# Kernel optimization log

Hardware: AMD Instinct MI355X
Metric: run time of the kernel (lower is better)

## Reference

```python
import jax, jax.numpy as jnp
import numpy as np

INPUT_SIZE = 512
HIDDEN_SIZE = 1024
OUTPUT_SIZE = 512
BATCH = 64
SEQ = 512


def _xavier(key, shape):
    fan_in, fan_out = shape
    bound = np.sqrt(6.0 / (fan_in + fan_out)).astype(np.float32)
    return jax.random.uniform(key, shape, jnp.float32, -bound, bound)


def setup_inputs() -> dict:
    key = jax.random.key(0)
    ks = jax.random.split(key, 7)
    comb = INPUT_SIZE + HIDDEN_SIZE
    return {
        "x": jax.random.normal(ks[0], (BATCH, SEQ, INPUT_SIZE), jnp.float32),
        "W_i": _xavier(ks[1], (comb, HIDDEN_SIZE)),
        "W_f": _xavier(ks[2], (comb, HIDDEN_SIZE)),
        "W_c": _xavier(ks[3], (comb, HIDDEN_SIZE)),
        "W_o": _xavier(ks[4], (comb, HIDDEN_SIZE)),
        "b_i": jnp.zeros((HIDDEN_SIZE,), jnp.float32),
        "b_f": jnp.zeros((HIDDEN_SIZE,), jnp.float32),
        "b_c": jnp.zeros((HIDDEN_SIZE,), jnp.float32),
        "b_o": jnp.zeros((HIDDEN_SIZE,), jnp.float32),
        "fc_w": _xavier(ks[5], (OUTPUT_SIZE, HIDDEN_SIZE)),  # torch Linear weight [out, in]
        "fc_b": jnp.zeros((OUTPUT_SIZE,), jnp.float32),
    }


def reference(x, W_i, W_f, W_c, W_o, b_i, b_f, b_c, b_o, fc_w, fc_b):
    batch = x.shape[0]
    hidden = W_i.shape[1]
    # Fuse the 4 gate weights into one [in+h, 4h] matrix: single GEMM per step.
    W = jnp.concatenate([W_i, W_f, W_c, W_o], axis=1)  # [in+h, 4h]
    b = jnp.concatenate([b_i, b_f, b_c, b_o], axis=0)  # [4h]

    def step(carry, x_t):
        h, c = carry
        combined = jnp.concatenate([x_t, h], axis=1)        # [B, in+h]
        gates = combined @ W + b                            # [B, 4h]
        i_t, f_t, g_t, o_t = jnp.split(gates, 4, axis=1)
        i_t = jax.nn.sigmoid(i_t)
        f_t = jax.nn.sigmoid(f_t)
        g_t = jnp.tanh(g_t)
        o_t = jax.nn.sigmoid(o_t)
        c = f_t * c + i_t * g_t
        h = o_t * jnp.tanh(c)
        return (h, c), None

    h0 = jnp.zeros((batch, hidden), x.dtype)
    c0 = jnp.zeros((batch, hidden), x.dtype)
    (h_T, _), _ = jax.lax.scan(step, (h0, c0), jnp.swapaxes(x, 0, 1))
    return h_T @ fc_w.T + fc_b  # [B, output_size]
```

## Files before the change

kernel.cpp:

```cpp
#include <hip/hip_runtime.h>

typedef unsigned char u8;
typedef unsigned short u16;
typedef unsigned int u32;
typedef unsigned long long u64;
typedef __attribute__((ext_vector_type(4))) int i32x4;
typedef __attribute__((ext_vector_type(4))) float f32x4;

#define SEQ 512

#define OFF_XBQ  0ull
#define OFF_WXQ  33554432ull
#define OFF_WHQ  35651584ull
#define OFF_SCL  39845888ull
#define OFF_SXG  39878656ull
#define OFF_HIMG 40009728ull
#define OFF_TAG  40271872ull
#define OFF_CTL  40305152ull

__device__ inline u16 f2bf(float f) {
  u32 u = __float_as_uint(f);
  return (u16)((u + 0x7fffu + ((u >> 16) & 1u)) >> 16);
}
__device__ inline float bf2f(u16 u) { return __uint_as_float(((u32)u) << 16); }
__device__ inline float sigm(float x) { return 1.f / (1.f + __expf(-x)); }
__device__ inline float tanh_(float x) { return 1.f - 2.f / (1.f + __expf(2.f * x)); }

#define MFMA_I8(a, b, c_) __builtin_amdgcn_mfma_i32_16x16x64_i8(a, b, c_, 0, 0, 0)

__device__ inline u32 ald32(const u32* p) {
  return __hip_atomic_load(p, __ATOMIC_RELAXED, __HIP_MEMORY_SCOPE_AGENT);
}
__device__ inline void st32_plain(u32* p, u32 v) {
  asm volatile("global_store_dword %0, %1, off" :: "v"(p), "v"(v) : "memory");
}
#define VMWAIT0() asm volatile("s_waitcnt vmcnt(0)" ::: "memory")
#define L1INV()   asm volatile("buffer_inv" ::: "memory")
#define CBAR()    asm volatile("" ::: "memory")

__global__ void pack_xq(const float* __restrict__ x, u8* __restrict__ xbq,
                        float* __restrict__ sxg) {
  __shared__ u8 st[1024];
  const int bid = blockIdx.x;
  const int brow = bid >> 9, tau = bid & 511;
  const int lane = threadIdx.x;
  const float* src = x + ((size_t)bid << 9) + lane * 8;
  float4 a = *(const float4*)src;
  float4 b = *(const float4*)(src + 4);
  float v[8] = {a.x, a.y, a.z, a.w, b.x, b.y, b.z, b.w};
  float m = 0.f;
#pragma unroll
  for (int j = 0; j < 8; ++j) m = fmaxf(m, fabsf(v[j]));
#pragma unroll
  for (int i = 1; i < 64; i <<= 1) m = fmaxf(m, __shfl_xor(m, i));
  m = fmaxf(m, 1e-20f);
  const float s = m * (1.f / 127.f), inv = 127.f / m;
#pragma unroll
  for (int j = 0; j < 8; ++j) {
    float t = v[j] * inv;
    float hi = rintf(t);
    float lo = rintf((t - hi) * 254.f);
    st[lane * 8 + j] = (u8)(signed char)(int)hi;
    st[512 + lane * 8 + j] = (u8)(signed char)(int)lo;
  }
  __syncthreads();
  const int hl = lane >> 5, ks = (lane >> 2) & 7, kg = lane & 3;
  uint4 u = *(const uint4*)&st[hl * 512 + ks * 64 + kg * 16];
  const int c = tau >> 2, tc = tau & 3, g = brow >> 3, rb = brow & 7;
  const int mrow = tc * 8 + rb, mt = mrow >> 4, m15 = mrow & 15;
  *(uint4*)(xbq + (size_t)(((((c * 8 + g) * 2 + hl) * 2 + mt) * 8 + ks) * 64 +
                           kg * 16 + m15) * 16) = u;
  if (lane == 0) sxg[tau * 64 + brow] = s;
}

__global__ void calc_scales(const float* __restrict__ W0, const float* __restrict__ W1,
                            const float* __restrict__ W2, const float* __restrict__ W3,
                            float* __restrict__ scl) {
  const int id = blockIdx.x * 256 + threadIdx.x;
  const int part = id >> 12, q = (id >> 10) & 3, cc = id & 1023;
  const float* Wg = q == 0 ? W0 : q == 1 ? W1 : q == 2 ? W2 : W3;
  const int r0 = part ? 512 : 0, n = part ? 1024 : 512;
  float mx = 1e-8f;
  for (int k = 0; k < n; ++k) mx = fmaxf(mx, fabsf(Wg[(size_t)(r0 + k) * 1024 + cc]));
  scl[id] = mx * (1.f / 127.f);
}

__global__ void pack_whq(const float* __restrict__ W0, const float* __restrict__ W1,
                         const float* __restrict__ W2, const float* __restrict__ W3,
                         const float* __restrict__ scl, u8* __restrict__ whq) {
  const int id = blockIdx.x * 256 + threadIdx.x;
  const int lane = id & 63, ks = (id >> 6) & 15, q = (id >> 10) & 3;
  const int w = (id >> 12) & 1, slot = id >> 13;
  const int hcol = slot * 32 + w * 16 + (lane & 15);
  const float* Wg = q == 0 ? W0 : q == 1 ? W1 : q == 2 ? W2 : W3;
  const int k0 = ks * 64 + (lane >> 4) * 16;
  const float inv_s = 1.f / scl[4096 + q * 1024 + hcol];
  u8 tmp[16];
#pragma unroll
  for (int j = 0; j < 16; ++j) {
    float v = Wg[(size_t)(512 + k0 + j) * 1024 + hcol] * inv_s;
    tmp[j] = (u8)(signed char)(int)rintf(fminf(fmaxf(v, -127.f), 127.f));
  }
  *(uint4*)(whq + (size_t)id * 16) = *(uint4*)tmp;
}

__global__ void pack_wxq(const float* __restrict__ W0, const float* __restrict__ W1,
                         const float* __restrict__ W2, const float* __restrict__ W3,
                         const float* __restrict__ scl, u8* __restrict__ wxq) {
  const int id = blockIdx.x * 256 + threadIdx.x;
  const int lane = id & 63, ks = (id >> 6) & 7, q = (id >> 9) & 3;
  const int w = (id >> 11) & 1, slot = id >> 12;
  const int hcol = slot * 32 + w * 16 + (lane & 15);
  const float* Wg = q == 0 ? W0 : q == 1 ? W1 : q == 2 ? W2 : W3;
  const int k0 = ks * 64 + (lane >> 4) * 16;
  const float inv_s = 1.f / scl[q * 1024 + hcol];
  u8 tmp[16];
#pragma unroll
  for (int j = 0; j < 16; ++j) {
    float v = Wg[(size_t)(k0 + j) * 1024 + hcol] * inv_s;
    tmp[j] = (u8)(signed char)(int)rintf(fminf(fmaxf(v, -127.f), 127.f));
  }
  *(uint4*)(wxq + (size_t)id * 16) = *(uint4*)tmp;
}

__global__ void __launch_bounds__(192, 1) lstm_main(
    char* __restrict__ ws,
    const float* __restrict__ b_i, const float* __restrict__ b_f,
    const float* __restrict__ b_c, const float* __restrict__ b_o,
    const float* __restrict__ fcw, const float* __restrict__ fcb,
    float* __restrict__ out) {
  __shared__ __align__(16) u8 wh[131072];
  __shared__ __align__(16) u16 ring_[8192];
  __shared__ __align__(16) u8 pub_[512];
  __shared__ u32 flg[16];

  const int tid = threadIdx.x;
  const int wid = tid >> 6;
  const int lane = tid & 63;
  const int kgrp = lane >> 4;
  const int l15 = lane & 15;

  u32 xcd;
  asm volatile("s_getreg_b32 %0, hwreg(HW_REG_XCC_ID, 0, 8)" : "=s"(xcd));
  const int g = (int)(xcd & 7);

  if (tid == 0) {
    u32 s = __hip_atomic_fetch_add((u32*)(ws + OFF_CTL) + g * 16, 1u,
                                   __ATOMIC_RELAXED, __HIP_MEMORY_SCOPE_SYSTEM);
    flg[0] = s; flg[1] = 0; flg[2] = 0; flg[3] = 0;
  }
  __syncthreads();
  const int slot = (int)flg[0];
  if (slot >= 32) return;

  u8* himg = (u8*)(ws + OFF_HIMG) + (size_t)g * 32768;
  u32* tags = (u32*)(ws + OFF_TAG) + g * 1024;
  const float* scl = (const float*)(ws + OFF_SCL);

  {
    const u8* src = (const u8*)(ws + OFF_WHQ) + (size_t)slot * 131072;
    for (int i = 0; i < 43; ++i) {
      int u = i * 192 + tid;
      if (u < 8192) *(uint4*)&wh[u * 16] = *(const uint4*)(src + u * 16);
    }
  }
  __syncthreads();

  if (wid == 2) {
    const u8* xq = (const u8*)(ws + OFF_XBQ);
    const u8* wxs = (const u8*)(ws + OFF_WXQ) + (size_t)slot * 65536;
    const float* sxg = (const float*)(ws + OFF_SXG);
    float swx[2][4], bs[2][4];
#pragma unroll
    for (int w2 = 0; w2 < 2; ++w2) {
      const int cwq = slot * 32 + w2 * 16 + l15;
#pragma unroll
      for (int q = 0; q < 4; ++q) swx[w2][q] = scl[q * 1024 + cwq];
      bs[w2][0] = b_i[cwq]; bs[w2][1] = b_f[cwq];
      bs[w2][2] = b_c[cwq]; bs[w2][3] = b_o[cwq];
    }
    for (int c = 0; c < 128; ++c) {
      if (c >= 2) {
        const u32 need = (u32)(4 * c - 4);
        while (((volatile u32*)flg)[2] < need || ((volatile u32*)flg)[3] < need) {}
        CBAR();
      }
      float sxv[2][4];
#pragma unroll
      for (int mt = 0; mt < 2; ++mt)
#pragma unroll
        for (int r = 0; r < 4; ++r)
          sxv[mt][r] = sxg[(c * 4 + mt * 2 + (kgrp >> 1)) * 64 + g * 8 + (kgrp & 1) * 4 + r];
      i32x4 accH[2][2][4], accL[2][2][4];
#pragma unroll
      for (int mt = 0; mt < 2; ++mt)
#pragma unroll
        for (int w2 = 0; w2 < 2; ++w2)
#pragma unroll
          for (int q = 0; q < 4; ++q) {
            accH[mt][w2][q] = (i32x4){0, 0, 0, 0};
            accL[mt][w2][q] = (i32x4){0, 0, 0, 0};
          }
      const u8* xc = xq + (size_t)(c * 8 + g) * 32768;
#pragma unroll 2
      for (int ks = 0; ks < 8; ++ks) {
        i32x4 aH0 = *(const i32x4*)(xc + (size_t)((0 * 2 + 0) * 8 + ks) * 1024 + lane * 16);
        i32x4 aH1 = *(const i32x4*)(xc + (size_t)((0 * 2 + 1) * 8 + ks) * 1024 + lane * 16);
        i32x4 aL0 = *(const i32x4*)(xc + (size_t)((1 * 2 + 0) * 8 + ks) * 1024 + lane * 16);
        i32x4 aL1 = *(const i32x4*)(xc + (size_t)((1 * 2 + 1) * 8 + ks) * 1024 + lane * 16);
#pragma unroll
        for (int w2 = 0; w2 < 2; ++w2)
#pragma unroll
          for (int q = 0; q < 4; ++q) {
            i32x4 b = *(const i32x4*)(wxs + (size_t)(((w2 * 4 + q) * 8 + ks) * 64 + lane) * 16);
            accH[0][w2][q] = MFMA_I8(aH0, b, accH[0][w2][q]);
            accH[1][w2][q] = MFMA_I8(aH1, b, accH[1][w2][q]);
            accL[0][w2][q] = MFMA_I8(aL0, b, accL[0][w2][q]);
            accL[1][w2][q] = MFMA_I8(aL1, b, accL[1][w2][q]);
          }
      }
#pragma unroll
      for (int mt = 0; mt < 2; ++mt)
#pragma unroll
        for (int w2 = 0; w2 < 2; ++w2)
#pragma unroll
          for (int q = 0; q < 4; ++q) {
            u64 pk = 0;
#pragma unroll
            for (int r = 0; r < 4; ++r) {
              float val = sxv[mt][r] * swx[w2][q] *
                          ((float)accH[mt][w2][q][r] + (float)accL[mt][w2][q][r] * (1.f / 254.f)) +
                          bs[w2][q];
              pk |= (u64)f2bf(val) << (16 * r);
            }
            const int tc = mt * 2 + (kgrp >> 1);
            const int cc2 = (w2 * 4 + q) * 16 + l15;
            const int rb0 = (kgrp & 1) * 4;
            *(u64*)&ring_[(((c & 1) * 4 + tc) * 128 + cc2) * 8 + rb0] = pk;
          }
      asm volatile("s_waitcnt lgkmcnt(0)" ::: "memory");
      ((volatile u32*)flg)[1] = (u32)(c + 1);
    }
    return;
  }

  const int w = wid;
  const int col = slot * 32 + w * 16 + l15;
  const int idx = slot * 2 + w;
  float sA[4];
#pragma unroll
  for (int q = 0; q < 4; ++q) sA[q] = scl[4096 + q * 1024 + col] * (1.f / 127.f);

  float cs[4] = {0.f, 0.f, 0.f, 0.f};
  u32* mytag = tags + idx * 16;
  const volatile u32* mypoll = (const volatile u32*)(tags + lane * 16);
  const int rbb = (kgrp & 1) * 4;

  for (int t = 1; t <= SEQ; ++t) {
    const int tau = t - 1, ch = tau >> 2, tc = tau & 3, par = tau & 1;
    while (((volatile u32*)flg)[1] <= (u32)ch) {}
    CBAR();
    f32x4 gx[4];
#pragma unroll
    for (int q = 0; q < 4; ++q) {
      u64 pk = *(const u64*)&ring_[(((ch & 1) * 4 + tc) * 128 + (w * 4 + q) * 16 + l15) * 8 + rbb];
      gx[q][0] = bf2f((u16)pk);         gx[q][1] = bf2f((u16)(pk >> 16));
      gx[q][2] = bf2f((u16)(pk >> 32)); gx[q][3] = bf2f((u16)(pk >> 48));
    }
    const u8* ab = himg + par * 16384 + lane * 16;
    u32 spins = 0;
    u64 rb = __ballot(*mypoll >= (u32)tau);
    i32x4 A[16];
    i32x4 acc[4];
#pragma unroll
    for (int q = 0; q < 4; ++q) acc[q] = (i32x4){0, 0, 0, 0};
#pragma unroll
    for (int q4 = 0; q4 < 4; ++q4) {
      const u64 need = 0xFFFFull << (q4 * 16);
      while ((rb & need) != need) {
        u32 v = (++spins > (1u << 20)) ? ald32((const u32*)mypoll) : *mypoll;
        rb = __ballot(v >= (u32)tau);
      }
      CBAR();
      L1INV();
#pragma unroll
      for (int k4 = 0; k4 < 4; ++k4)
        A[q4 * 4 + k4] = *(const i32x4*)(ab + (size_t)(q4 * 4 + k4) * 1024);
      if (q4 > 0) {
#pragma unroll
        for (int k4 = 0; k4 < 4; ++k4) {
          const int ks = (q4 - 1) * 4 + k4;
#pragma unroll
          for (int q = 0; q < 4; ++q) {
            i32x4 b = *(const i32x4*)&wh[(size_t)(((w * 4 + q) * 16 + ks) * 64 + lane) * 16];
            acc[q] = MFMA_I8(A[ks], b, acc[q]);
          }
        }
      }
    }
#pragma unroll
    for (int k4 = 0; k4 < 4; ++k4) {
      const int ks = 12 + k4;
#pragma unroll
      for (int q = 0; q < 4; ++q) {
        i32x4 b = *(const i32x4*)&wh[(size_t)(((w * 4 + q) * 16 + ks) * 64 + lane) * 16];
        acc[q] = MFMA_I8(A[ks], b, acc[q]);
      }
    }
#pragma unroll
    for (int r = 0; r < 4; ++r) {
      float p[4];
#pragma unroll
      for (int q = 0; q < 4; ++q) {
        float hiF = (float)acc[q][r];
        float loF = (float)__shfl_xor(acc[q][r], 32);
        p[q] = fmaf(sA[q], fmaf(loF, 1.f / 254.f, hiF), gx[q][r]);
      }
      float iv = sigm(p[0]), fv = sigm(p[1]), gv = tanh_(p[2]), ov = sigm(p[3]);
      float cn = fv * cs[r] + iv * gv;
      cs[r] = cn;
      float h = ov * tanh_(cn);
      float hq = h * 127.f;
      float hi = rintf(hq);
      float lo = rintf((hq - hi) * 254.f);
      if (kgrp < 2) {
        const int rr = kgrp * 4 + r;
        pub_[w * 256 + rr * 16 + l15] = (u8)(signed char)(int)hi;
        pub_[w * 256 + (8 + rr) * 16 + l15] = (u8)(signed char)(int)lo;
      }
    }
    asm volatile("s_waitcnt lgkmcnt(0)" ::: "memory");
    if (lane < 16) {
      uint4 v = *(const uint4*)&pub_[w * 256 + lane * 16];
      u8* dst = himg + (size_t)((t & 1) * 16384) +
                (size_t)(((idx >> 2) * 64 + (idx & 3) * 16 + lane) * 16);
      *(uint4*)dst = v;
    }
    VMWAIT0();
    if (lane == 0) st32_plain(mytag, (u32)t);
    ((volatile u32*)flg)[2 + w] = (u32)t;
  }

  {
    u32 spins = 0;
    u64 rb = __ballot(*mypoll >= (u32)SEQ);
    while (rb != ~0ull) {
      u32 v = (++spins > (1u << 20)) ? ald32((const u32*)mypoll) : *mypoll;
      rb = __ballot(v >= (u32)SEQ);
    }
  }
  CBAR();
  L1INV();
  {
    const int row = tid >> 4, c16 = tid & 15;
    const int ocol = slot * 16 + c16;
    const float* wr = fcw + (size_t)ocol * 1024;
    float acc = fcb[ocol];
    const float C1 = 1.f / 127.f, C2 = 1.f / 32258.f;
    for (int ks = 0; ks < 16; ++ks) {
#pragma unroll
      for (int kg = 0; kg < 4; ++kg) {
        union { i32x4 v; signed char b[16]; } H, L;
        H.v = *(const i32x4*)(himg + (size_t)((ks * 64 + kg * 16 + row) * 16));
        L.v = *(const i32x4*)(himg + (size_t)((ks * 64 + kg * 16 + 8 + row) * 16));
        const float* wp = wr + ks * 64 + kg * 16;
#pragma unroll
        for (int j = 0; j < 16; ++j)
          acc += ((float)H.b[j] * C1 + (float)L.b[j] * C2) * wp[j];
      }
    }
    out[(size_t)(g * 8 + row) * 512 + ocol] = acc;
  }
}

extern "C" void kernel_launch(void* const* d_in, const int* in_sizes, int n_in,
                              void* d_out, int out_size, void* d_ws, size_t ws_size,
                              hipStream_t stream) {
  const float* x  = (const float*)d_in[0];
  const float* W0 = (const float*)d_in[1];
  const float* W1 = (const float*)d_in[2];
  const float* W2 = (const float*)d_in[3];
  const float* W3 = (const float*)d_in[4];
  const float* bi = (const float*)d_in[5];
  const float* bf = (const float*)d_in[6];
  const float* bc = (const float*)d_in[7];
  const float* bo = (const float*)d_in[8];
  const float* fcw = (const float*)d_in[9];
  const float* fcb = (const float*)d_in[10];
  float* out = (float*)d_out;

  char* ws = (char*)d_ws;
  pack_xq<<<dim3(32768), dim3(64), 0, stream>>>(x, (u8*)(ws + OFF_XBQ),
                                                (float*)(ws + OFF_SXG));
  calc_scales<<<dim3(32), dim3(256), 0, stream>>>(W0, W1, W2, W3, (float*)(ws + OFF_SCL));
  pack_whq<<<dim3(1024), dim3(256), 0, stream>>>(W0, W1, W2, W3,
                                                 (const float*)(ws + OFF_SCL),
                                                 (u8*)(ws + OFF_WHQ));
  pack_wxq<<<dim3(512), dim3(256), 0, stream>>>(W0, W1, W2, W3,
                                                (const float*)(ws + OFF_SCL),
                                                (u8*)(ws + OFF_WXQ));
  hipMemsetAsync(ws + OFF_HIMG, 0, 262144 + 32768 + 1024, stream);
  lstm_main<<<dim3(256), dim3(192), 0, stream>>>(ws, bi, bf, bc, bo, fcw, fcb, out);
}
```

Measured before the change: 1.835 ms.

## Fast-path full-ready MFMA, exp2/rcp activations, direct byte stores, sleep in producer wait

Pre-scales the gate inputs by log2(e) so sigmoid and tanh can use the hardware exp2 and rcp builtins. Hoists the readiness ballot ahead of the ring wait and adds a fast path that loads all 16 A chunks and runs the MFMAs back-to-back when every producer has already published. Drops the LDS staging buffer and writes the hi/lo h bytes straight to global memory, and makes the x-gate producer wave sleep while spinning. The byte-granular global stores replace 16-byte coalesced stores and may add memory traffic on the critical path. s_sleep may also delay how quickly the producer wave notices progress.

```diff
diff --git a/kernel.cpp b/kernel.cpp
--- a/kernel.cpp
+++ b/kernel.cpp
@@ -8,6 +8,8 @@
 typedef __attribute__((ext_vector_type(4))) float f32x4;
 
 #define SEQ 512
+#define L2E  1.4426950408889634f
+#define L2E2 2.8853900817779268f
 
 #define OFF_XBQ  0ull
 #define OFF_WXQ  33554432ull
@@ -23,8 +25,19 @@
   return (u16)((u + 0x7fffu + ((u >> 16) & 1u)) >> 16);
 }
 __device__ inline float bf2f(u16 u) { return __uint_as_float(((u32)u) << 16); }
-__device__ inline float sigm(float x) { return 1.f / (1.f + __expf(-x)); }
-__device__ inline float tanh_(float x) { return 1.f - 2.f / (1.f + __expf(2.f * x)); }
+
+#if __has_builtin(__builtin_amdgcn_exp2f)
+#define EXP2(x) __builtin_amdgcn_exp2f(x)
+#else
+#define EXP2(x) exp2f(x)
+#endif
+#if __has_builtin(__builtin_amdgcn_rcpf)
+#define RCP(x) __builtin_amdgcn_rcpf(x)
+#else
+#define RCP(x) (1.f / (x))
+#endif
+__device__ inline float sigm2(float p) { return RCP(1.f + EXP2(-p)); }
+__device__ inline float tanh2(float p) { return 1.f - 2.f * RCP(1.f + EXP2(p)); }
 
 #define MFMA_I8(a, b, c_) __builtin_amdgcn_mfma_i32_16x16x64_i8(a, b, c_, 0, 0, 0)
 
@@ -131,7 +144,6 @@
     float* __restrict__ out) {
   __shared__ __align__(16) u8 wh[131072];
   __shared__ __align__(16) u16 ring_[8192];
-  __shared__ __align__(16) u8 pub_[512];
   __shared__ u32 flg[16];
 
   const int tid = threadIdx.x;
@@ -175,14 +187,18 @@
     for (int w2 = 0; w2 < 2; ++w2) {
       const int cwq = slot * 32 + w2 * 16 + l15;
 #pragma unroll
-      for (int q = 0; q < 4; ++q) swx[w2][q] = scl[q * 1024 + cwq];
-      bs[w2][0] = b_i[cwq]; bs[w2][1] = b_f[cwq];
-      bs[w2][2] = b_c[cwq]; bs[w2][3] = b_o[cwq];
+      for (int q = 0; q < 4; ++q) {
+        const float sc = (q == 2) ? L2E2 : L2E;
+        swx[w2][q] = scl[q * 1024 + cwq] * sc;
+      }
+      bs[w2][0] = b_i[cwq] * L2E;  bs[w2][1] = b_f[cwq] * L2E;
+      bs[w2][2] = b_c[cwq] * L2E2; bs[w2][3] = b_o[cwq] * L2E;
     }
     for (int c = 0; c < 128; ++c) {
       if (c >= 2) {
         const u32 need = (u32)(4 * c - 4);
-        while (((volatile u32*)flg)[2] < need || ((volatile u32*)flg)[3] < need) {}
+        while (((volatile u32*)flg)[2] < need || ((volatile u32*)flg)[3] < need)
+          __builtin_amdgcn_s_sleep(1);
         CBAR();
       }
       float sxv[2][4];
@@ -249,15 +265,18 @@
   const int idx = slot * 2 + w;
   float sA[4];
 #pragma unroll
-  for (int q = 0; q < 4; ++q) sA[q] = scl[4096 + q * 1024 + col] * (1.f / 127.f);
+  for (int q = 0; q < 4; ++q)
+    sA[q] = scl[4096 + q * 1024 + col] * (1.f / 127.f) * ((q == 2) ? L2E2 : L2E);
 
   float cs[4] = {0.f, 0.f, 0.f, 0.f};
   u32* mytag = tags + idx * 16;
   const volatile u32* mypoll = (const volatile u32*)(tags + lane * 16);
   const int rbb = (kgrp & 1) * 4;
+  u8* const pubbase = himg + (size_t)(((idx >> 2) * 64 + (idx & 3) * 16) * 16);
 
   for (int t = 1; t <= SEQ; ++t) {
     const int tau = t - 1, ch = tau >> 2, tc = tau & 3, par = tau & 1;
+    u64 rb = __ballot(*mypoll >= (u32)tau);
     while (((volatile u32*)flg)[1] <= (u32)ch) {}
     CBAR();
     f32x4 gx[4];
@@ -268,45 +287,60 @@
       gx[q][2] = bf2f((u16)(pk >> 32)); gx[q][3] = bf2f((u16)(pk >> 48));
     }
     const u8* ab = himg + par * 16384 + lane * 16;
-    u32 spins = 0;
-    u64 rb = __ballot(*mypoll >= (u32)tau);
     i32x4 A[16];
     i32x4 acc[4];
 #pragma unroll
     for (int q = 0; q < 4; ++q) acc[q] = (i32x4){0, 0, 0, 0};
-#pragma unroll
-    for (int q4 = 0; q4 < 4; ++q4) {
-      const u64 need = 0xFFFFull << (q4 * 16);
-      while ((rb & need) != need) {
-        u32 v = (++spins > (1u << 20)) ? ald32((const u32*)mypoll) : *mypoll;
-        rb = __ballot(v >= (u32)tau);
-      }
+    if (rb == ~0ull) {
       CBAR();
       L1INV();
 #pragma unroll
-      for (int k4 = 0; k4 < 4; ++k4)
-        A[q4 * 4 + k4] = *(const i32x4*)(ab + (size_t)(q4 * 4 + k4) * 1024);
-      if (q4 > 0) {
-#pragma unroll
-        for (int k4 = 0; k4 < 4; ++k4) {
-          const int ks = (q4 - 1) * 4 + k4;
-#pragma unroll
-          for (int q = 0; q < 4; ++q) {
-            i32x4 b = *(const i32x4*)&wh[(size_t)(((w * 4 + q) * 16 + ks) * 64 + lane) * 16];
-            acc[q] = MFMA_I8(A[ks], b, acc[q]);
+      for (int ks = 0; ks < 16; ++ks)
+        A[ks] = *(const i32x4*)(ab + (size_t)ks * 1024);
+#pragma unroll
+      for (int ks = 0; ks < 16; ++ks)
+#pragma unroll
+        for (int q = 0; q < 4; ++q) {
+          i32x4 b = *(const i32x4*)&wh[(size_t)(((w * 4 + q) * 16 + ks) * 64 + lane) * 16];
+          acc[q] = MFMA_I8(A[ks], b, acc[q]);
+        }
+    } else {
+      u32 spins = 0;
+#pragma unroll
+      for (int q4 = 0; q4 < 4; ++q4) {
+        const u64 need = 0xFFFFull << (q4 * 16);
+        while ((rb & need) != need) {
+          u32 v = (++spins > (1u << 20)) ? ald32((const u32*)mypoll) : *mypoll;
+          rb = __ballot(v >= (u32)tau);
+        }
+        CBAR();
+        L1INV();
+#pragma unroll
+        for (int k4 = 0; k4 < 4; ++k4)
+          A[q4 * 4 + k4] = *(const i32x4*)(ab + (size_t)(q4 * 4 + k4) * 1024);
+        if (q4 > 0) {
+#pragma unroll
+          for (int k4 = 0; k4 < 4; ++k4) {
+            const int ks = (q4 - 1) * 4 + k4;
+#pragma unroll
+            for (int q = 0; q < 4; ++q) {
+              i32x4 b = *(const i32x4*)&wh[(size_t)(((w * 4 + q) * 16 + ks) * 64 + lane) * 16];
+              acc[q] = MFMA_I8(A[ks], b, acc[q]);
+            }
           }
         }
       }
-    }
-#pragma unroll
-    for (int k4 = 0; k4 < 4; ++k4) {
-      const int ks = 12 + k4;
-#pragma unroll
-      for (int q = 0; q < 4; ++q) {
-        i32x4 b = *(const i32x4*)&wh[(size_t)(((w * 4 + q) * 16 + ks) * 64 + lane) * 16];
-        acc[q] = MFMA_I8(A[ks], b, acc[q]);
-      }
-    }
+#pragma unroll
+      for (int k4 = 0; k4 < 4; ++k4) {
+        const int ks = 12 + k4;
+#pragma unroll
+        for (int q = 0; q < 4; ++q) {
+          i32x4 b = *(const i32x4*)&wh[(size_t)(((w * 4 + q) * 16 + ks) * 64 + lane) * 16];
+          acc[q] = MFMA_I8(A[ks], b, acc[q]);
+        }
+      }
+    }
+    u8* dstT = pubbase + (size_t)((t & 1) * 16384);
 #pragma unroll
     for (int r = 0; r < 4; ++r) {
       float p[4];
@@ -316,25 +350,18 @@
         float loF = (float)__shfl_xor(acc[q][r], 32);
         p[q] = fmaf(sA[q], fmaf(loF, 1.f / 254.f, hiF), gx[q][r]);
       }
-      float iv = sigm(p[0]), fv = sigm(p[1]), gv = tanh_(p[2]), ov = sigm(p[3]);
+      float iv = sigm2(p[0]), fv = sigm2(p[1]), gv = tanh2(p[2]), ov = sigm2(p[3]);
       float cn = fv * cs[r] + iv * gv;
       cs[r] = cn;
-      float h = ov * tanh_(cn);
+      float h = ov * tanh2(cn * L2E2);
       float hq = h * 127.f;
       float hi = rintf(hq);
       float lo = rintf((hq - hi) * 254.f);
       if (kgrp < 2) {
         const int rr = kgrp * 4 + r;
-        pub_[w * 256 + rr * 16 + l15] = (u8)(signed char)(int)hi;
-        pub_[w * 256 + (8 + rr) * 16 + l15] = (u8)(signed char)(int)lo;
-      }
-    }
-    asm volatile("s_waitcnt lgkmcnt(0)" ::: "memory");
-    if (lane < 16) {
-      uint4 v = *(const uint4*)&pub_[w * 256 + lane * 16];
-      u8* dst = himg + (size_t)((t & 1) * 16384) +
-                (size_t)(((idx >> 2) * 64 + (idx & 3) * 16 + lane) * 16);
-      *(uint4*)dst = v;
+        dstT[rr * 16 + l15] = (u8)(signed char)(int)hi;
+        dstT[rr * 16 + 128 + l15] = (u8)(signed char)(int)lo;
+      }
     }
     VMWAIT0();
     if (lane == 0) st32_plain(mytag, (u32)t);
```

After: 1.661 ms. 1.1x faster.
